# Kernel tuning notes

Hardware: AMD Instinct MI355X
Metric: run time of the kernel (lower is better)

The kernel has to match this reference:

```python
import jax, jax.numpy as jnp
import numpy as np

DIM = 512
T = 65536


def setup_inputs() -> dict:
    key = jax.random.key(0)
    k1, = jax.random.split(key, 1)
    z_rest = jax.random.normal(k1, (T, DIM), dtype=jnp.float32)
    # var_vbl = inv_softplus(sqrt(var_init)) with var_init=1.0 -> log(expm1(1.0))
    var_vbl = jnp.full((DIM,), float(np.log(np.expm1(1.0))), dtype=jnp.float32)
    # corr_vbl = inv_sigmoid(0.1) = log(0.1) - log(0.9)
    corr_vbl = jnp.full((DIM,), float(np.log(0.1) - np.log(0.9)), dtype=jnp.float32)
    prior_mu = jnp.zeros((DIM,), dtype=jnp.float32)
    return {"z_rest": z_rest, "var_vbl": var_vbl, "corr_vbl": corr_vbl, "prior_mu": prior_mu}


def reference(z_rest, var_vbl, corr_vbl, prior_mu):
    # init_train_lkd with z_context=None, starting from fresh state (sample_size=0).
    prior_var = jnp.square(jax.nn.softplus(var_vbl))          # [D]
    prior_cov = jax.nn.sigmoid(corr_vbl) * prior_var          # [D]
    two_pi = 2.0 * jnp.pi

    def step(carry, xs):
        mu, var, lkd = carry
        z, t = xs  # z: [D], t: scalar step index (== sample_size - 1 after increment)
        lkd = lkd + jnp.sum(-0.5 * jnp.log(two_pi * var)
                            - jnp.square(z - mu) / (2.0 * var))
        dd = prior_cov / (prior_var + prior_cov * t)
        mu = (1.0 - dd) * mu + z * dd
        var = (1.0 - dd) * var + (prior_var - prior_cov) * dd
        return (mu, var, lkd), None

    ts = jnp.arange(z_rest.shape[0], dtype=z_rest.dtype)
    init = (prior_mu.astype(z_rest.dtype), prior_var, jnp.zeros((), z_rest.dtype))
    (_, _, lkd), _ = jax.lax.scan(step, init, (z_rest, ts))
    return lkd
```

## Files before the change

### kernel.cpp

```cpp
#include <hip/hip_runtime.h>
#include <math.h>


#define DIM    512
#define TT     65536
#define CHUNKS 1024
#define ROWS   64
#define GROUPS 64
#define CPG    16

#define TWO_PI 6.283185307179586

__global__ __launch_bounds__(128) void k1_fused(const float* __restrict__ z,
                                                const float* __restrict__ var_vbl,
                                                const float* __restrict__ corr_vbl,
                                                const float* __restrict__ prior_mu,
                                                float* __restrict__ sums,
                                                float* __restrict__ s0a,
                                                float* __restrict__ s1a,
                                                float* __restrict__ s2a) {
    const int chunk = blockIdx.x;
    const int tid = threadIdx.x;
    const int d0 = tid * 4;
    const float t0m1 = (float)(chunk * ROWS) - 1.0f;

    float vv[4], cc[4], k0[4], L[4], S0[4], S1[4], S2[4], Dprev[4], invDprev[4];
#pragma unroll
    for (int j = 0; j < 4; ++j) {
        const int d = d0 + j;
        float spv = log1pf(expf(var_vbl[d]));
        float v = spv * spv;
        float c = v / (1.0f + expf(-corr_vbl[d]));
        vv[j] = v;
        cc[j] = c;
        k0[j] = (v - c) * prior_mu[d];
        L[j] = 0.f; S0[j] = 0.f; S1[j] = 0.f; S2[j] = 0.f;
        Dprev[j] = fmaf(c, t0m1, v);
        invDprev[j] = __builtin_amdgcn_rcpf(Dprev[j]);
    }

    const float4* zp = reinterpret_cast<const float4*>(z)
                       + (size_t)chunk * ROWS * (DIM / 4) + tid;
    float tf = t0m1 + 1.0f;
#pragma unroll 4
    for (int r = 0; r < ROWS; ++r) {
        float4 zv = zp[(size_t)r * (DIM / 4)];
        float zz[4] = {zv.x, zv.y, zv.z, zv.w};
#pragma unroll
        for (int j = 0; j < 4; ++j) {
            float Dt = fmaf(cc[j], tf, vv[j]);
            float invDt = __builtin_amdgcn_rcpf(Dt);
            float w = fmaf(Dprev[j], zz[j], -fmaf(cc[j], L[j], k0[j]));
            float rr = invDt * invDprev[j];
            S0[j] += rr;
            float rw = rr * w;
            S1[j] += rw;
            S2[j] = fmaf(rw, w, S2[j]);
            L[j] += zz[j];
            Dprev[j] = Dt;
            invDprev[j] = invDt;
        }
        tf += 1.0f;
    }

    const size_t o4 = (size_t)chunk * (DIM / 4) + tid;
    reinterpret_cast<float4*>(sums)[o4] = make_float4(L[0], L[1], L[2], L[3]);
    reinterpret_cast<float4*>(s0a)[o4] = make_float4(S0[0], S0[1], S0[2], S0[3]);
    reinterpret_cast<float4*>(s1a)[o4] = make_float4(S1[0], S1[1], S1[2], S1[3]);
    reinterpret_cast<float4*>(s2a)[o4] = make_float4(S2[0], S2[1], S2[2], S2[3]);
}

__global__ __launch_bounds__(512) void k2_combine(const float* __restrict__ sums,
                                                  const float* __restrict__ s0a,
                                                  const float* __restrict__ s1a,
                                                  const float* __restrict__ s2a,
                                                  const float* __restrict__ var_vbl,
                                                  const float* __restrict__ corr_vbl,
                                                  float* __restrict__ out) {
    const int g = blockIdx.x;
    const int d = threadIdx.x;
    float spv = log1pf(expf(var_vbl[d]));
    float v = spv * spv;
    float c = v / (1.0f + expf(-corr_vbl[d]));
    float kq = 0.5f / (v - c);

    float run = 0.f;
    const int nrows = g * CPG;
#pragma unroll 8
    for (int i = 0; i < nrows; ++i)
        run += sums[(size_t)i * DIM + d];

    float q = 0.f;
#pragma unroll
    for (int i = 0; i < CPG; ++i) {
        const size_t idx = (size_t)(g * CPG + i) * DIM + d;
        float s = sums[idx];
        float S0 = s0a[idx];
        float S1 = s1a[idx];
        float S2 = s2a[idx];
        float cP = c * run;
        q += kq * (S2 - 2.f * cP * S1 + cP * cP * S0);
        run += s;
    }

    for (int off = 32; off > 0; off >>= 1) q += __shfl_down(q, off, 64);
    __shared__ float wsred[8];
    const int lane = d & 63, w = d >> 6;
    if (lane == 0) wsred[w] = q;
    __syncthreads();
    if (d == 0) {
        float tot = 0.f;
#pragma unroll
        for (int i = 0; i < 8; ++i) tot += wsred[i];
        atomicAdd(out, -tot);
    }

    if (g == 0) {
        double sp = log1p(exp((double)var_vbl[d]));
        double vd = sp * sp;
        double cd = vd / (1.0 + exp(-(double)corr_vbl[d]));
        double vmc = vd - cd;
        double Dlast = vd + cd * (double)(TT - 1);
        double Ld = -0.5 * ((double)TT * (log(TWO_PI) + log(vmc)) + log(Dlast / vmc));
        __shared__ double redd[512];
        redd[d] = Ld;
        __syncthreads();
        for (int s = 256; s > 0; s >>= 1) {
            if (d < s) redd[d] += redd[d + s];
            __syncthreads();
        }
        if (d == 0) atomicAdd(out, (float)redd[0]);
    }
}

extern "C" void kernel_launch(void* const* d_in, const int* in_sizes, int n_in,
                              void* d_out, int out_size, void* d_ws, size_t ws_size,
                              hipStream_t stream) {
    const float* z = (const float*)d_in[0];
    const float* var_vbl = (const float*)d_in[1];
    const float* corr_vbl = (const float*)d_in[2];
    const float* prior_mu = (const float*)d_in[3];
    float* out = (float*)d_out;
    float* sums = (float*)d_ws;
    float* s0a = sums + (size_t)CHUNKS * DIM;
    float* s1a = s0a + (size_t)CHUNKS * DIM;
    float* s2a = s1a + (size_t)CHUNKS * DIM;

    hipMemsetAsync(d_out, 0, sizeof(float), stream);
    k1_fused<<<CHUNKS, 128, 0, stream>>>(z, var_vbl, corr_vbl, prior_mu,
                                         sums, s0a, s1a, s2a);
    k2_combine<<<GROUPS, 512, 0, stream>>>(sums, s0a, s1a, s2a,
                                           var_vbl, corr_vbl, out);
}
```

Baseline: 246.6 us.

## Compute S0 analytically, add group-sum prefix kernel, drop memset

The per-chunk S0 accumulator is replaced by a closed form: a telescoping sum of 1/(D_{t-1} D_t), computed in the combine kernel from the chunk endpoints. This removes one accumulator and one output array from the main kernel. The serial prefix over up to 1024 chunk rows in the combine step becomes a two-level scheme, with a new kernel building per-group sums. That kernel also writes the constant term directly, so the memset is no longer needed. The cost is an extra kernel launch, and the closed form for S0 may lose some float precision compared with direct summation.

```diff
diff --git a/kernel.cpp b/kernel.cpp
--- a/kernel.cpp
+++ b/kernel.cpp
@@ -16,7 +16,6 @@
                                                 const float* __restrict__ corr_vbl,
                                                 const float* __restrict__ prior_mu,
                                                 float* __restrict__ sums,
-                                                float* __restrict__ s0a,
                                                 float* __restrict__ s1a,
                                                 float* __restrict__ s2a) {
     const int chunk = blockIdx.x;
@@ -24,7 +23,7 @@
     const int d0 = tid * 4;
     const float t0m1 = (float)(chunk * ROWS) - 1.0f;
 
-    float vv[4], cc[4], k0[4], L[4], S0[4], S1[4], S2[4], Dprev[4], invDprev[4];
+    float vv[4], cc[4], k0[4], L[4], S1[4], S2[4], Dprev[4], invDprev[4];
 #pragma unroll
     for (int j = 0; j < 4; ++j) {
         const int d = d0 + j;
@@ -34,7 +33,7 @@
         vv[j] = v;
         cc[j] = c;
         k0[j] = (v - c) * prior_mu[d];
-        L[j] = 0.f; S0[j] = 0.f; S1[j] = 0.f; S2[j] = 0.f;
+        L[j] = 0.f; S1[j] = 0.f; S2[j] = 0.f;
         Dprev[j] = fmaf(c, t0m1, v);
         invDprev[j] = __builtin_amdgcn_rcpf(Dprev[j]);
     }
@@ -51,9 +50,7 @@
             float Dt = fmaf(cc[j], tf, vv[j]);
             float invDt = __builtin_amdgcn_rcpf(Dt);
             float w = fmaf(Dprev[j], zz[j], -fmaf(cc[j], L[j], k0[j]));
-            float rr = invDt * invDprev[j];
-            S0[j] += rr;
-            float rw = rr * w;
+            float rw = (invDt * invDprev[j]) * w;
             S1[j] += rw;
             S2[j] = fmaf(rw, w, S2[j]);
             L[j] += zz[j];
@@ -65,39 +62,74 @@
 
     const size_t o4 = (size_t)chunk * (DIM / 4) + tid;
     reinterpret_cast<float4*>(sums)[o4] = make_float4(L[0], L[1], L[2], L[3]);
-    reinterpret_cast<float4*>(s0a)[o4] = make_float4(S0[0], S0[1], S0[2], S0[3]);
     reinterpret_cast<float4*>(s1a)[o4] = make_float4(S1[0], S1[1], S1[2], S1[3]);
     reinterpret_cast<float4*>(s2a)[o4] = make_float4(S2[0], S2[1], S2[2], S2[3]);
 }
 
-__global__ __launch_bounds__(512) void k2_combine(const float* __restrict__ sums,
-                                                  const float* __restrict__ s0a,
-                                                  const float* __restrict__ s1a,
-                                                  const float* __restrict__ s2a,
-                                                  const float* __restrict__ var_vbl,
-                                                  const float* __restrict__ corr_vbl,
-                                                  float* __restrict__ out) {
+__global__ __launch_bounds__(512) void k2a_gsum(const float* __restrict__ sums,
+                                                float* __restrict__ gsums,
+                                                const float* __restrict__ var_vbl,
+                                                const float* __restrict__ corr_vbl,
+                                                float* __restrict__ out) {
+    const int g = blockIdx.x;
+    const int d = threadIdx.x;
+    if (g < GROUPS) {
+        float vals[CPG];
+#pragma unroll
+        for (int i = 0; i < CPG; ++i)
+            vals[i] = sums[(size_t)(g * CPG + i) * DIM + d];
+        float run = 0.f;
+#pragma unroll
+        for (int i = 0; i < CPG; ++i) run += vals[i];
+        gsums[(size_t)g * DIM + d] = run;
+    } else {
+        double sp = log1p(exp((double)var_vbl[d]));
+        double vd = sp * sp;
+        double cd = vd / (1.0 + exp(-(double)corr_vbl[d]));
+        double vmc = vd - cd;
+        double Dlast = vd + cd * (double)(TT - 1);
+        double Ld = -0.5 * ((double)TT * (log(TWO_PI) + log(vmc)) + log(Dlast / vmc));
+        __shared__ double redd[512];
+        redd[d] = Ld;
+        __syncthreads();
+        for (int s = 256; s > 0; s >>= 1) {
+            if (d < s) redd[d] += redd[d + s];
+            __syncthreads();
+        }
+        if (d == 0) out[0] = (float)redd[0];
+    }
+}
+
+__global__ __launch_bounds__(512) void k2b_combine(const float* __restrict__ sums,
+                                                   const float* __restrict__ s1a,
+                                                   const float* __restrict__ s2a,
+                                                   const float* __restrict__ gsums,
+                                                   const float* __restrict__ var_vbl,
+                                                   const float* __restrict__ corr_vbl,
+                                                   float* __restrict__ out) {
     const int g = blockIdx.x;
     const int d = threadIdx.x;
     float spv = log1pf(expf(var_vbl[d]));
     float v = spv * spv;
     float c = v / (1.0f + expf(-corr_vbl[d]));
     float kq = 0.5f / (v - c);
+    float invc = 1.0f / c;
 
     float run = 0.f;
-    const int nrows = g * CPG;
-#pragma unroll 8
-    for (int i = 0; i < nrows; ++i)
-        run += sums[(size_t)i * DIM + d];
+#pragma unroll 16
+    for (int i = 0; i < g; ++i) run += gsums[(size_t)i * DIM + d];
 
     float q = 0.f;
 #pragma unroll
     for (int i = 0; i < CPG; ++i) {
-        const size_t idx = (size_t)(g * CPG + i) * DIM + d;
+        const int ch = g * CPG + i;
+        const size_t idx = (size_t)ch * DIM + d;
         float s = sums[idx];
-        float S0 = s0a[idx];
         float S1 = s1a[idx];
         float S2 = s2a[idx];
+        float Ds = fmaf(c, (float)(ch * ROWS) - 1.0f, v);
+        float De = fmaf(c, (float)(ch * ROWS + ROWS - 1), v);
+        float S0 = (1.0f / Ds - 1.0f / De) * invc;
         float cP = c * run;
         q += kq * (S2 - 2.f * cP * S1 + cP * cP * S0);
         run += s;
@@ -114,23 +146,6 @@
         for (int i = 0; i < 8; ++i) tot += wsred[i];
         atomicAdd(out, -tot);
     }
-
-    if (g == 0) {
-        double sp = log1p(exp((double)var_vbl[d]));
-        double vd = sp * sp;
-        double cd = vd / (1.0 + exp(-(double)corr_vbl[d]));
-        double vmc = vd - cd;
-        double Dlast = vd + cd * (double)(TT - 1);
-        double Ld = -0.5 * ((double)TT * (log(TWO_PI) + log(vmc)) + log(Dlast / vmc));
-        __shared__ double redd[512];
-        redd[d] = Ld;
-        __syncthreads();
-        for (int s = 256; s > 0; s >>= 1) {
-            if (d < s) redd[d] += redd[d + s];
-            __syncthreads();
-        }
-        if (d == 0) atomicAdd(out, (float)redd[0]);
-    }
 }
 
 extern "C" void kernel_launch(void* const* d_in, const int* in_sizes, int n_in,
@@ -142,13 +157,13 @@
     const float* prior_mu = (const float*)d_in[3];
     float* out = (float*)d_out;
     float* sums = (float*)d_ws;
-    float* s0a = sums + (size_t)CHUNKS * DIM;
-    float* s1a = s0a + (size_t)CHUNKS * DIM;
+    float* s1a = sums + (size_t)CHUNKS * DIM;
     float* s2a = s1a + (size_t)CHUNKS * DIM;
+    float* gsums = s2a + (size_t)CHUNKS * DIM;
 
-    hipMemsetAsync(d_out, 0, sizeof(float), stream);
     k1_fused<<<CHUNKS, 128, 0, stream>>>(z, var_vbl, corr_vbl, prior_mu,
-                                         sums, s0a, s1a, s2a);
-    k2_combine<<<GROUPS, 512, 0, stream>>>(sums, s0a, s1a, s2a,
-                                           var_vbl, corr_vbl, out);
+                                         sums, s1a, s2a);
+    k2a_gsum<<<GROUPS + 1, 512, 0, stream>>>(sums, gsums, var_vbl, corr_vbl, out);
+    k2b_combine<<<GROUPS, 512, 0, stream>>>(sums, s1a, s2a, gsums,
+                                            var_vbl, corr_vbl, out);
 }
```

Measured after the change: 209.7 us. 1.18x faster.
